# Optimization experiments

Measured on AMD Instinct MI355X. Metric: run time of the kernel, lower is better.

## Reference

```python
import jax, jax.numpy as jnp
import numpy as np
from jax import lax

# db4 decomposition low-pass filter (pywt convention, ascending index)
DEC_LO = np.array([-0.010597401784997278, 0.032883011666982945, 0.030841381835986965,
                   -0.18703481171888114, -0.02798376941698385, 0.6308807679295904,
                   0.7148465705525415, 0.23037781330885523], dtype=np.float32)
L = 8
REC_LO = DEC_LO[::-1].copy()
DEC_HI = (REC_LO * ((-1.0) ** (np.arange(L) + 1))).astype(np.float32)
REC_HI = DEC_HI[::-1].copy()


def _dwt_last(x, lo, hi):
    """Single-level DWT along last axis, pywt 'symmetric' mode.
    Returns (cA, cD), each (..., (N+L-1)//2)."""
    ext = jnp.pad(x, [(0, 0)] * (x.ndim - 1) + [(L - 1, L - 1)], mode='symmetric')[..., 1:]
    z = ext.reshape(-1, 1, ext.shape[-1])
    # correlation with flipped filter == true convolution
    k = jnp.stack([lo[::-1], hi[::-1]])[:, None, :]  # (2,1,L)
    y = lax.conv_general_dilated(z, k, (2,), 'VALID', dimension_numbers=('NCH', 'OIH', 'NCH'))
    y = y.reshape(x.shape[:-1] + (2, y.shape[-1]))
    return y[..., 0, :], y[..., 1, :]


def _idwt_last(cA, cD, lo, hi):
    """Single-level inverse DWT along last axis (pywt upsampling convolution)."""
    n = cA.shape[-1]
    up = jnp.zeros(cA.shape[:-1] + (2, 2 * n - 1), cA.dtype)
    up = up.at[..., 0, ::2].set(cA).at[..., 1, ::2].set(cD)
    z = up.reshape(-1, 2, 2 * n - 1)
    k = jnp.stack([lo[::-1], hi[::-1]])[None, :, :]  # (1,2,L) -> sum of lo/hi branches
    y = lax.conv_general_dilated(z, k, (1,), [(L - 1, L - 1)], dimension_numbers=('NCH', 'OIH', 'NCH'))
    y = y[:, 0, L - 2: 2 * n]  # length 2n - L + 2
    return y.reshape(cA.shape[:-1] + (2 * n - L + 2,))


def dwt2d(x):
    lo, hi = jnp.asarray(DEC_LO), jnp.asarray(DEC_HI)
    a, d = _dwt_last(x, lo, hi)                       # along W
    aa, da = _dwt_last(a.swapaxes(-1, -2), lo, hi)    # along H
    ad, dd = _dwt_last(d.swapaxes(-1, -2), lo, hi)
    LL = aa.swapaxes(-1, -2)
    LH = da.swapaxes(-1, -2)   # cH: detail along H, approx along W
    HL = ad.swapaxes(-1, -2)   # cV: approx along H, detail along W
    HH = dd.swapaxes(-1, -2)
    return LL, LH, HL, HH


def idwt2d(LL, LH, HL, HH):
    lo, hi = jnp.asarray(REC_LO), jnp.asarray(REC_HI)
    a = _idwt_last(LL.swapaxes(-1, -2), LH.swapaxes(-1, -2), lo, hi).swapaxes(-1, -2)  # along H
    d = _idwt_last(HL.swapaxes(-1, -2), HH.swapaxes(-1, -2), lo, hi).swapaxes(-1, -2)
    return _idwt_last(a, d, lo, hi)  # along W


def attention_weight(x, c1w, c1b, c2w, gamma, beta, rmean, rvar):
    """x: (b, w, c, h). Max/mean pool over dim 1, 1x1 conv 2->1, depthwise conv1d
    over c channels, BatchNorm1d (eval), sigmoid gate."""
    feat = jnp.stack([x.max(axis=1), x.mean(axis=1)], axis=1)  # (b,2,c,h)
    y = jnp.einsum('i,bich->bch', c1w.reshape(2), feat) + c1b[0]  # (b,c,h)
    C = y.shape[1]
    p = (c2w.shape[-1] - 1) // 2
    y = lax.conv_general_dilated(y, c2w, (1,), [(p, p)], feature_group_count=C,
                                 dimension_numbers=('NCH', 'OIH', 'NCH'))
    y = (y - rmean[:, None]) * lax.rsqrt(rvar[:, None] + 1e-5) * gamma[:, None] + beta[:, None]
    return x * jax.nn.sigmoid(y)[:, None]


def _forward(x, lh_c1w, lh_c1b, lh_c2w, lh_g, lh_b, lh_m, lh_v,
             hl_c1w, hl_c1b, hl_c2w, hl_g, hl_b, hl_m, hl_v):
    LL, LH, HL, HH = dwt2d(x)
    LHp = attention_weight(LH.transpose(0, 3, 1, 2), lh_c1w, lh_c1b, lh_c2w, lh_g, lh_b, lh_m, lh_v).transpose(0, 2, 3, 1)
    HLp = attention_weight(HL.transpose(0, 2, 1, 3), hl_c1w, hl_c1b, hl_c2w, hl_g, hl_b, hl_m, hl_v).transpose(0, 2, 1, 3)
    rec = idwt2d(LL, LHp, HLp, HH)
    H, W = x.shape[-2], x.shape[-1]
    return x + rec[..., :H, :W]


def setup_inputs() -> dict:
    key = jax.random.key(0)
    ks = jax.random.split(key, 16)
    B, C, H, W, K = 8, 64, 512, 512, 3
    d = {"x": jax.random.normal(ks[0], (B, C, H, W), dtype=jnp.float32)}
    for i, pre in enumerate(["lh", "hl"]):
        base = 1 + 7 * i
        d[pre + "_c1w"] = jax.random.normal(ks[base + 0], (1, 2, 1, 1), dtype=jnp.float32) * 0.5
        d[pre + "_c1b"] = jax.random.normal(ks[base + 1], (1,), dtype=jnp.float32) * 0.1
        d[pre + "_c2w"] = jax.random.normal(ks[base + 2], (C, 1, K), dtype=jnp.float32) * 0.3
        d[pre + "_g"] = jnp.ones((C,), dtype=jnp.float32)
        d[pre + "_b"] = jnp.zeros((C,), dtype=jnp.float32)
        d[pre + "_m"] = jax.random.normal(ks[base + 3], (C,), dtype=jnp.float32) * 0.1
        d[pre + "_v"] = jax.random.uniform(ks[base + 4], (C,), dtype=jnp.float32, minval=0.5, maxval=1.5)
    return d


def reference(x, lh_c1w, lh_c1b, lh_c2w, lh_g, lh_b, lh_m, lh_v,
              hl_c1w, hl_c1b, hl_c2w, hl_g, hl_b, hl_m, hl_v):
    return _forward(x, lh_c1w, lh_c1b, lh_c2w, lh_g, lh_b, lh_m, lh_v,
                    hl_c1w, hl_c1b, hl_c2w, hl_g, hl_b, hl_m, hl_v)
```

## Files before the change

### kernel.cpp

```cpp
#include <hip/hip_runtime.h>

typedef _Float16 h16;
typedef _Float16 h16x2 __attribute__((ext_vector_type(2)));
typedef _Float16 h16x4 __attribute__((ext_vector_type(4)));
typedef _Float16 h16x8 __attribute__((ext_vector_type(8)));
typedef float f32x4 __attribute__((ext_vector_type(4)));

#define N_IMG 512
#define C_CH  64
#define H_IN  512
#define W_IN  512
#define NC    259
#define PITH  264
#define S_IMGH ((size_t)NC * PITH)
#define NSB    ((size_t)N_IMG * S_IMGH)
#define GPIT  264
#define FSTRIP 17
#define LROWS  38

constexpr float DLO[8] = {
  -0.010597401784997278f,  0.032883011666982945f,  0.030841381835986965f, -0.18703481171888114f,
  -0.02798376941698385f,   0.6308807679295904f,    0.7148465705525415f,    0.23037781330885523f};
constexpr float DHI[8] = {
  -0.23037781330885523f,   0.7148465705525415f,   -0.6308807679295904f,   -0.02798376941698385f,
   0.18703481171888114f,   0.030841381835986965f, -0.032883011666982945f, -0.010597401784997278f};
constexpr float RLO[8] = {
   0.23037781330885523f,   0.7148465705525415f,    0.6308807679295904f,   -0.02798376941698385f,
  -0.18703481171888114f,   0.030841381835986965f,  0.032883011666982945f, -0.010597401784997278f};
constexpr float RHI[8] = {
  -0.010597401784997278f, -0.032883011666982945f,  0.030841381835986965f,  0.18703481171888114f,
  -0.02798376941698385f,  -0.6308807679295904f,    0.7148465705525415f,   -0.23037781330885523f};

__global__ __launch_bounds__(512) void k_fwd(const float* __restrict__ x,
                                             h16* __restrict__ wsh,
                                             float* __restrict__ stat) {
  __shared__ h16 sa16[LROWS * PITH];
  __shared__ h16 sd16[LROWS * PITH];
  const int p = blockIdx.x;
  const int w = (p & 7) * 1088 + (p >> 3);
  const int bc = w / FSTRIP;
  const int bx = w - bc * FSTRIP;
  const int h0 = bx * 16;
  const int hcount = min(16, NC - h0);
  const int nrows = 2 * hcount + 6;
  const int tid = threadIdx.x;
  const int wave = tid >> 6, lane = tid & 63;
  const float* xim = x + (size_t)bc * (H_IN * (size_t)W_IN);

  for (int j = wave; j < nrows; j += 8) {
    int r = 2 * h0 - 6 + j;
    r = r < 0 ? -r - 1 : (r >= H_IN ? 2 * H_IN - 1 - r : r);
    const float* xrow = xim + (size_t)r * W_IN;
    h16* saj = sa16 + j * PITH;
    h16* sdj = sd16 + j * PITH;
    const int base = lane ? 8 * lane - 8 : 0;
    const float4 q0 = *(const float4*)(xrow + base);
    const float4 q1 = *(const float4*)(xrow + base + 4);
    const float4 q2 = *(const float4*)(xrow + base + 8);
    const float4 q3 = *(const float4*)(xrow + base + 12);
    const float v[16] = {q0.x, q0.y, q0.z, q0.w, q1.x, q1.y, q1.z, q1.w,
                         q2.x, q2.y, q2.z, q2.w, q3.x, q3.y, q3.z, q3.w};
    float A[4], D[4];
    if (lane == 0) {
#pragma unroll
      for (int i = 0; i < 4; ++i) {
        float a = 0.f, d = 0.f;
#pragma unroll
        for (int m = 0; m < 8; ++m) {
          int pp = 2 * i + 1 - m; pp = pp < 0 ? -pp - 1 : pp;
          const float t = v[pp];
          a += DLO[m] * t; d += DHI[m] * t;
        }
        A[i] = a; D[i] = d;
      }
      h16x4 oa, od;
#pragma unroll
      for (int k = 0; k < 4; ++k) { oa[k] = (h16)A[k]; od[k] = (h16)D[k]; }
      *(h16x4*)(saj) = oa; *(h16x4*)(sdj) = od;
    } else {
#pragma unroll
      for (int k = 0; k < 4; ++k) {
        float a = 0.f, d = 0.f;
#pragma unroll
        for (int m = 0; m < 8; ++m) {
          const float t = v[2 * k + 9 - m];
          a += DLO[m] * t; d += DHI[m] * t;
        }
        A[k] = a; D[k] = d;
      }
      h16x4 oa, od;
#pragma unroll
      for (int k = 0; k < 4; ++k) { oa[k] = (h16)A[k]; od[k] = (h16)D[k]; }
      *(h16x4*)(saj + 4 * lane) = oa; *(h16x4*)(sdj + 4 * lane) = od;
      if (lane == 63) {
#pragma unroll
        for (int i = 256; i < 259; ++i) {
          float a = 0.f, d = 0.f;
#pragma unroll
          for (int m = 0; m < 8; ++m) {
            int pp = 2 * i + 1 - m; pp = pp >= 512 ? 1023 - pp : pp;
            const float t = v[pp - 496];
            a += DLO[m] * t; d += DHI[m] * t;
          }
          saj[i] = (h16)a; sdj[i] = (h16)d;
        }
      }
    }
  }
  __syncthreads();

  h16* __restrict__ LHp = wsh;
  h16* __restrict__ HLp = wsh + NSB;
  const size_t obase = (size_t)bc * S_IMGH;
  const int ntask = hcount * 65;
  float rlh[3][4], rhl[3][4];
#pragma unroll
  for (int slot = 0; slot < 3; ++slot) {
    const int task = tid + slot * 512;
    if (task < ntask) {
      const int dh = task / 65, pq = task - dh * 65;
      const int i0 = 4 * pq;
      float lh[4] = {0, 0, 0, 0}, hl[4] = {0, 0, 0, 0};
#pragma unroll
      for (int m = 0; m < 8; ++m) {
        const int j = 2 * dh + 7 - m;
        const h16x4 av = *(const h16x4*)(sa16 + j * PITH + i0);
        const h16x4 dv = *(const h16x4*)(sd16 + j * PITH + i0);
        lh[0] += DHI[m] * (float)av[0]; lh[1] += DHI[m] * (float)av[1];
        lh[2] += DHI[m] * (float)av[2]; lh[3] += DHI[m] * (float)av[3];
        hl[0] += DLO[m] * (float)dv[0]; hl[1] += DLO[m] * (float)dv[1];
        hl[2] += DLO[m] * (float)dv[2]; hl[3] += DLO[m] * (float)dv[3];
      }
      if (i0 == 256) { lh[3] = 0.f; hl[3] = 0.f; }
      const size_t ob = obase + (size_t)(h0 + dh) * PITH + i0;
      h16x4 o;
      o[0] = (h16)lh[0]; o[1] = (h16)lh[1]; o[2] = (h16)lh[2]; o[3] = (h16)lh[3];
      *(h16x4*)(LHp + ob) = o;
      o[0] = (h16)hl[0]; o[1] = (h16)hl[1]; o[2] = (h16)hl[2]; o[3] = (h16)hl[3];
      *(h16x4*)(HLp + ob) = o;
#pragma unroll
      for (int k = 0; k < 4; ++k) { rlh[slot][k] = lh[k]; rhl[slot][k] = hl[k]; }
    }
  }
  __syncthreads();

  float* scol = (float*)sa16;
  float* prmx = (float*)sd16;
  float* prsm = prmx + 1056;
#pragma unroll
  for (int slot = 0; slot < 3; ++slot) {
    const int task = tid + slot * 512;
    if (task < ntask) {
      const int dh = task / 65, pq = task - dh * 65;
      *(float4*)(scol + dh * 264 + 4 * pq) = {rhl[slot][0], rhl[slot][1], rhl[slot][2], rhl[slot][3]};
      const float m01 = fmaxf(rlh[slot][0], rlh[slot][1]);
      const float m23 = (pq == 64) ? rlh[slot][2] : fmaxf(rlh[slot][2], rlh[slot][3]);
      prmx[task] = fmaxf(m01, m23);
      prsm[task] = rlh[slot][0] + rlh[slot][1] + rlh[slot][2] + rlh[slot][3];
    }
  }
  __syncthreads();
  float* rsM = stat;
  float* rsS = stat + (size_t)N_IMG * 264;
  float* cpM = rsS + (size_t)N_IMG * 264;
  float* cpS = cpM + (size_t)N_IMG * FSTRIP * 264;
  for (int hh = wave; hh < hcount; hh += 8) {
    float m = prmx[hh * 65 + lane], s = prsm[hh * 65 + lane];
    if (lane == 0) { m = fmaxf(m, prmx[hh * 65 + 64]); s += prsm[hh * 65 + 64]; }
#pragma unroll
    for (int off = 32; off; off >>= 1) {
      m = fmaxf(m, __shfl_xor(m, off)); s += __shfl_xor(s, off);
    }
    if (lane == 0) {
      rsM[bc * 264 + h0 + hh] = m;
      rsS[bc * 264 + h0 + hh] = s;
    }
  }
  if (tid < 264) {
    float m = -3.4e38f, s = 0.f;
    for (int dh = 0; dh < hcount; ++dh) {
      const float vv = scol[dh * 264 + tid]; m = fmaxf(m, vv); s += vv;
    }
    const size_t cb = ((size_t)bc * FSTRIP + bx) * 264 + tid;
    cpM[cb] = m; cpS[cb] = s;
  }
}

__global__ __launch_bounds__(256) void k_gate(
    const float* __restrict__ stat, float* __restrict__ gout,
    const float* lc1w, const float* lc1b, const float* lc2w,
    const float* lg, const float* lb, const float* lm, const float* lv,
    const float* hc1w, const float* hc1b, const float* hc2w,
    const float* hg, const float* hb, const float* hm, const float* hv) {
  __shared__ float cmx[264], csm[264], y0a[264], y0b[264];
  const int bc = blockIdx.x;
  const int tid = threadIdx.x;
  const float* rsM = stat;
  const float* rsS = stat + (size_t)N_IMG * 264;
  const float* cpM = rsS + (size_t)N_IMG * 264;
  const float* cpS = cpM + (size_t)N_IMG * FSTRIP * 264;

  for (int col = tid; col < 264; col += 256) {
    float m = -3.4e38f, s = 0.f;
    for (int st = 0; st < FSTRIP; ++st) {
      const size_t cb = ((size_t)bc * FSTRIP + st) * 264 + col;
      m = fmaxf(m, cpM[cb]); s += cpS[cb];
    }
    cmx[col] = m; csm[col] = s;
  }
  __syncthreads();
  const float lw0 = lc1w[0], lw1 = lc1w[1], lbb0 = lc1b[0];
  const float hw0 = hc1w[0], hw1 = hc1w[1], hbb0 = hc1b[0];
  for (int idx = tid; idx < NC; idx += 256) {
    y0a[idx] = lw0 * rsM[bc * 264 + idx] + lw1 * (rsS[bc * 264 + idx] * (1.f / NC)) + lbb0;
    y0b[idx] = hw0 * cmx[idx] + hw1 * (csm[idx] * (1.f / NC)) + hbb0;
  }
  __syncthreads();
  const int c = bc & (C_CH - 1);
  const float lk0 = lc2w[c * 3], lk1 = lc2w[c * 3 + 1], lk2 = lc2w[c * 3 + 2];
  const float hk0 = hc2w[c * 3], hk1 = hc2w[c * 3 + 1], hk2 = hc2w[c * 3 + 2];
  const float lsc = rsqrtf(lv[c] + 1e-5f) * lg[c], lmu = lm[c], lbe = lb[c];
  const float hsc = rsqrtf(hv[c] + 1e-5f) * hg[c], hmu = hm[c], hbe = hb[c];
  for (int idx = tid; idx < NC; idx += 256) {
    float a = idx > 0 ? y0a[idx - 1] : 0.f;
    float b = y0a[idx];
    float d = idx < NC - 1 ? y0a[idx + 1] : 0.f;
    float y = lk0 * a + lk1 * b + lk2 * d;
    y = (y - lmu) * lsc + lbe;
    gout[(size_t)bc * GPIT + idx] = 1.f / (1.f + expf(-y)) - 1.f;

    a = idx > 0 ? y0b[idx - 1] : 0.f;
    b = y0b[idx];
    d = idx < NC - 1 ? y0b[idx + 1] : 0.f;
    y = hk0 * a + hk1 * b + hk2 * d;
    y = (y - hmu) * hsc + hbe;
    gout[(size_t)N_IMG * GPIT + (size_t)bc * GPIT + idx] = 1.f / (1.f + expf(-y)) - 1.f;
  }
}

__global__ __launch_bounds__(512) void k_inv(const h16* __restrict__ wsh,
                                             const float* __restrict__ gbuf,
                                             const float* __restrict__ x,
                                             float* __restrict__ out) {
  __shared__ float sB[7][PITH], sC[7][PITH];
  __shared__ float a2[8][PITH], d2[8][PITH];
  __shared__ float sghl[PITH];
  const int p = blockIdx.x;
  const int w = (p & 7) * 4096 + (p >> 3);
  const int bc = w >> 6;
  const int t0 = (w & 63) * 8;
  const int u0 = t0 >> 1;
  const int tid = threadIdx.x;
  const h16* LHh = wsh       + (size_t)bc * S_IMGH;
  const h16* HLh = wsh + NSB + (size_t)bc * S_IMGH;
  const float* glh = gbuf + (size_t)bc * GPIT;
  const float* ghl = gbuf + (size_t)N_IMG * GPIT + (size_t)bc * GPIT;

  if (tid < 66) *(float4*)(sghl + 4 * tid) = *(const float4*)(ghl + 4 * tid);

  for (int q = tid; q < 7 * 33; q += 512) {
    const int j = q / 33, b8 = (q - j * 33) * 8;
    const int u = u0 + j;
    const float gl = glh[u];
    const size_t rb = (size_t)u * PITH + b8;
    const h16x8 Bv = *(const h16x8*)(LHh + rb);
    const h16x8 Cv = *(const h16x8*)(HLh + rb);
    float4 f0 = {(float)Bv[0] * gl, (float)Bv[1] * gl, (float)Bv[2] * gl, (float)Bv[3] * gl};
    float4 f1 = {(float)Bv[4] * gl, (float)Bv[5] * gl, (float)Bv[6] * gl, (float)Bv[7] * gl};
    *(float4*)(&sB[j][b8]) = f0; *(float4*)(&sB[j][b8 + 4]) = f1;
    f0 = {(float)Cv[0], (float)Cv[1], (float)Cv[2], (float)Cv[3]};
    f1 = {(float)Cv[4], (float)Cv[5], (float)Cv[6], (float)Cv[7]};
    *(float4*)(&sC[j][b8]) = f0; *(float4*)(&sC[j][b8 + 4]) = f1;
  }
  __syncthreads();

  for (int task = tid; task < 8 * 132; task += 512) {
    const int dt = task / 132, pq = task - dt * 132;
    const int i = 2 * pq;
    const int par = dt & 1, lj0 = dt >> 1;
    float ax = 0.f, ay = 0.f, dx_ = 0.f, dy_ = 0.f;
#pragma unroll
    for (int jj = 0; jj < 4; ++jj) {
      const int lj = lj0 + 3 - jj;
      const float rh = par ? RHI[1 + 2 * jj] : RHI[2 * jj];
      const float rl = par ? RLO[1 + 2 * jj] : RLO[2 * jj];
      const float2 b_ = *(const float2*)(&sB[lj][i]);
      const float2 c_ = *(const float2*)(&sC[lj][i]);
      ax += b_.x * rh; ay += b_.y * rh;
      dx_ += c_.x * rl; dy_ += c_.y * rl;
    }
    *(float2*)(&a2[dt][i]) = {ax, ay};
    *(float2*)(&d2[dt][i]) = {sghl[i] * dx_, sghl[i + 1] * dy_};
  }
  __syncthreads();

  for (int task = tid; task < 8 * 128; task += 512) {
    const int dt = task >> 7, r = task & 127;
    const int q = 2 * r;
    const float a_[5] = {a2[dt][q], a2[dt][q + 1], a2[dt][q + 2], a2[dt][q + 3], a2[dt][q + 4]};
    const float d_[5] = {d2[dt][q], d2[dt][q + 1], d2[dt][q + 2], d2[dt][q + 3], d2[dt][q + 4]};
    float vv[4];
#pragma unroll
    for (int k = 0; k < 4; ++k) {
      float s = 0.f;
      const int base = k >> 1, par = k & 1;
#pragma unroll
      for (int jj = 0; jj < 4; ++jj)
        s += a_[base + 3 - jj] * RLO[par + 2 * jj] + d_[base + 3 - jj] * RHI[par + 2 * jj];
      vv[k] = s;
    }
    const size_t orow = ((size_t)bc * H_IN + (size_t)(t0 + dt)) * W_IN + 4 * r;
    const f32x4 xv = __builtin_nontemporal_load((const f32x4*)(x + orow));
    f32x4 ov;
    ov.x = 2.f * xv.x + vv[0]; ov.y = 2.f * xv.y + vv[1];
    ov.z = 2.f * xv.z + vv[2]; ov.w = 2.f * xv.w + vv[3];
    __builtin_nontemporal_store(ov, (f32x4*)(out + orow));
  }
}

extern "C" void kernel_launch(void* const* d_in, const int* in_sizes, int n_in,
                              void* d_out, int out_size, void* d_ws, size_t ws_size,
                              hipStream_t stream) {
  const float* x = (const float*)d_in[0];
  h16* wsh = (h16*)d_ws;
  float* statf = (float*)(wsh + 2 * NSB);
  float* gbuf = statf + 2 * (size_t)N_IMG * 264 + 2 * (size_t)N_IMG * FSTRIP * 264;
  float* out = (float*)d_out;

  k_fwd<<<dim3(FSTRIP * N_IMG), 512, 0, stream>>>(x, wsh, statf);
  k_gate<<<dim3(N_IMG), 256, 0, stream>>>(
      statf, gbuf,
      (const float*)d_in[1], (const float*)d_in[2], (const float*)d_in[3],
      (const float*)d_in[4], (const float*)d_in[5], (const float*)d_in[6], (const float*)d_in[7],
      (const float*)d_in[8], (const float*)d_in[9], (const float*)d_in[10],
      (const float*)d_in[11], (const float*)d_in[12], (const float*)d_in[13], (const float*)d_in[14]);
  k_inv<<<dim3(64 * N_IMG), 512, 0, stream>>>(wsh, gbuf, x, out);
}
```

Measured before the change: 405.8 us.

## Interleave LH/HL subbands in fp16 pairs and use packed half math

Stores the two detail subbands interleaved as half2 pairs in one workspace buffer and one shared tile. Forward and inverse filtering now run with packed fp16 vector multiply-adds and fdot2 instead of scalar fp32. The inverse kernel handles 16 output rows per block instead of 8, with intermediates kept in fp16 shared memory. This is meant to cut ALU work, shared memory footprint and the number of load instructions, and to reuse halo rows across more outputs. In exchange, fp16 accumulation lowers precision of the intermediate sums.

```diff
diff --git a/kernel.cpp b/kernel.cpp
--- a/kernel.cpp
+++ b/kernel.cpp
@@ -6,14 +6,21 @@
 typedef _Float16 h16x8 __attribute__((ext_vector_type(8)));
 typedef float f32x4 __attribute__((ext_vector_type(4)));
 
+#if __has_builtin(__builtin_amdgcn_fdot2)
+#define FDOT2(a, b, c) __builtin_amdgcn_fdot2((a), (b), (c), false)
+#else
+static __device__ __forceinline__ float FDOT2(h16x2 a, h16x2 b, float c) {
+  return c + (float)a[0] * (float)b[0] + (float)a[1] * (float)b[1];
+}
+#endif
+
 #define N_IMG 512
 #define C_CH  64
 #define H_IN  512
 #define W_IN  512
 #define NC    259
-#define PITH  264
-#define S_IMGH ((size_t)NC * PITH)
-#define NSB    ((size_t)N_IMG * S_IMGH)
+#define PITP  528
+#define S2    ((size_t)NC * PITP)
 #define GPIT  264
 #define FSTRIP 17
 #define LROWS  38
@@ -34,8 +41,7 @@
 __global__ __launch_bounds__(512) void k_fwd(const float* __restrict__ x,
                                              h16* __restrict__ wsh,
                                              float* __restrict__ stat) {
-  __shared__ h16 sa16[LROWS * PITH];
-  __shared__ h16 sd16[LROWS * PITH];
+  __shared__ h16 sad[LROWS * PITP];
   const int p = blockIdx.x;
   const int w = (p & 7) * 1088 + (p >> 3);
   const int bc = w / FSTRIP;
@@ -51,8 +57,7 @@
     int r = 2 * h0 - 6 + j;
     r = r < 0 ? -r - 1 : (r >= H_IN ? 2 * H_IN - 1 - r : r);
     const float* xrow = xim + (size_t)r * W_IN;
-    h16* saj = sa16 + j * PITH;
-    h16* sdj = sd16 + j * PITH;
+    h16* sj = sad + j * PITP;
     const int base = lane ? 8 * lane - 8 : 0;
     const float4 q0 = *(const float4*)(xrow + base);
     const float4 q1 = *(const float4*)(xrow + base + 4);
@@ -60,8 +65,8 @@
     const float4 q3 = *(const float4*)(xrow + base + 12);
     const float v[16] = {q0.x, q0.y, q0.z, q0.w, q1.x, q1.y, q1.z, q1.w,
                          q2.x, q2.y, q2.z, q2.w, q3.x, q3.y, q3.z, q3.w};
-    float A[4], D[4];
     if (lane == 0) {
+      h16x8 o;
 #pragma unroll
       for (int i = 0; i < 4; ++i) {
         float a = 0.f, d = 0.f;
@@ -71,13 +76,11 @@
           const float t = v[pp];
           a += DLO[m] * t; d += DHI[m] * t;
         }
-        A[i] = a; D[i] = d;
-      }
-      h16x4 oa, od;
-#pragma unroll
-      for (int k = 0; k < 4; ++k) { oa[k] = (h16)A[k]; od[k] = (h16)D[k]; }
-      *(h16x4*)(saj) = oa; *(h16x4*)(sdj) = od;
+        o[2 * i] = (h16)a; o[2 * i + 1] = (h16)d;
+      }
+      *(h16x8*)(sj) = o;
     } else {
+      h16x8 o;
 #pragma unroll
       for (int k = 0; k < 4; ++k) {
         float a = 0.f, d = 0.f;
@@ -86,12 +89,9 @@
           const float t = v[2 * k + 9 - m];
           a += DLO[m] * t; d += DHI[m] * t;
         }
-        A[k] = a; D[k] = d;
-      }
-      h16x4 oa, od;
-#pragma unroll
-      for (int k = 0; k < 4; ++k) { oa[k] = (h16)A[k]; od[k] = (h16)D[k]; }
-      *(h16x4*)(saj + 4 * lane) = oa; *(h16x4*)(sdj + 4 * lane) = od;
+        o[2 * k] = (h16)a; o[2 * k + 1] = (h16)d;
+      }
+      *(h16x8*)(sj + 8 * lane) = o;
       if (lane == 63) {
 #pragma unroll
         for (int i = 256; i < 259; ++i) {
@@ -102,61 +102,64 @@
             const float t = v[pp - 496];
             a += DLO[m] * t; d += DHI[m] * t;
           }
-          saj[i] = (h16)a; sdj[i] = (h16)d;
+          h16x2 o2; o2[0] = (h16)a; o2[1] = (h16)d;
+          *(h16x2*)(sj + 2 * i) = o2;
         }
       }
     }
   }
   __syncthreads();
 
-  h16* __restrict__ LHp = wsh;
-  h16* __restrict__ HLp = wsh + NSB;
-  const size_t obase = (size_t)bc * S_IMGH;
-  const int ntask = hcount * 65;
+  const size_t obase = (size_t)bc * S2;
+  const int ntask = hcount * 66;
   float rlh[3][4], rhl[3][4];
 #pragma unroll
   for (int slot = 0; slot < 3; ++slot) {
     const int task = tid + slot * 512;
     if (task < ntask) {
-      const int dh = task / 65, pq = task - dh * 65;
-      const int i0 = 4 * pq;
-      float lh[4] = {0, 0, 0, 0}, hl[4] = {0, 0, 0, 0};
+      const int dh = task / 66, pq = task - dh * 66;
+      h16x2 a0 = {0, 0}, a1 = {0, 0}, a2_ = {0, 0}, a3 = {0, 0};
 #pragma unroll
       for (int m = 0; m < 8; ++m) {
         const int j = 2 * dh + 7 - m;
-        const h16x4 av = *(const h16x4*)(sa16 + j * PITH + i0);
-        const h16x4 dv = *(const h16x4*)(sd16 + j * PITH + i0);
-        lh[0] += DHI[m] * (float)av[0]; lh[1] += DHI[m] * (float)av[1];
-        lh[2] += DHI[m] * (float)av[2]; lh[3] += DHI[m] * (float)av[3];
-        hl[0] += DLO[m] * (float)dv[0]; hl[1] += DLO[m] * (float)dv[1];
-        hl[2] += DLO[m] * (float)dv[2]; hl[3] += DLO[m] * (float)dv[3];
-      }
-      if (i0 == 256) { lh[3] = 0.f; hl[3] = 0.f; }
-      const size_t ob = obase + (size_t)(h0 + dh) * PITH + i0;
-      h16x4 o;
-      o[0] = (h16)lh[0]; o[1] = (h16)lh[1]; o[2] = (h16)lh[2]; o[3] = (h16)lh[3];
-      *(h16x4*)(LHp + ob) = o;
-      o[0] = (h16)hl[0]; o[1] = (h16)hl[1]; o[2] = (h16)hl[2]; o[3] = (h16)hl[3];
-      *(h16x4*)(HLp + ob) = o;
-#pragma unroll
-      for (int k = 0; k < 4; ++k) { rlh[slot][k] = lh[k]; rhl[slot][k] = hl[k]; }
-    }
-  }
-  __syncthreads();
-
-  float* scol = (float*)sa16;
-  float* prmx = (float*)sd16;
+        const h16x8 pr = *(const h16x8*)(sad + j * PITP + 8 * pq);
+        const h16x2 cf = {(h16)DHI[m], (h16)DLO[m]};
+        const h16x2 p0 = {pr[0], pr[1]}, p1 = {pr[2], pr[3]};
+        const h16x2 p2 = {pr[4], pr[5]}, p3 = {pr[6], pr[7]};
+        a0 += cf * p0; a1 += cf * p1; a2_ += cf * p2; a3 += cf * p3;
+      }
+      if (pq == 64) { a3 = (h16x2){0, 0}; }
+      if (pq == 65) { a0 = a1 = a2_ = a3 = (h16x2){0, 0}; }
+      h16x8 o = {a0[0], a0[1], a1[0], a1[1], a2_[0], a2_[1], a3[0], a3[1]};
+      *(h16x8*)(wsh + obase + (size_t)(h0 + dh) * PITP + 8 * pq) = o;
+      rlh[slot][0] = (float)a0[0]; rlh[slot][1] = (float)a1[0];
+      rlh[slot][2] = (float)a2_[0]; rlh[slot][3] = (float)a3[0];
+      rhl[slot][0] = (float)a0[1]; rhl[slot][1] = (float)a1[1];
+      rhl[slot][2] = (float)a2_[1]; rhl[slot][3] = (float)a3[1];
+    }
+  }
+  __syncthreads();
+
+  float* scol = (float*)sad;
+  float* prmx = scol + 16 * 264;
   float* prsm = prmx + 1056;
 #pragma unroll
   for (int slot = 0; slot < 3; ++slot) {
     const int task = tid + slot * 512;
     if (task < ntask) {
-      const int dh = task / 65, pq = task - dh * 65;
-      *(float4*)(scol + dh * 264 + 4 * pq) = {rhl[slot][0], rhl[slot][1], rhl[slot][2], rhl[slot][3]};
-      const float m01 = fmaxf(rlh[slot][0], rlh[slot][1]);
-      const float m23 = (pq == 64) ? rlh[slot][2] : fmaxf(rlh[slot][2], rlh[slot][3]);
-      prmx[task] = fmaxf(m01, m23);
-      prsm[task] = rlh[slot][0] + rlh[slot][1] + rlh[slot][2] + rlh[slot][3];
+      const int dh = task / 66, pq = task - dh * 66;
+      if (pq < 66) {
+        *(float4*)(scol + dh * 264 + 4 * pq) =
+            {rhl[slot][0], rhl[slot][1], rhl[slot][2], rhl[slot][3]};
+      }
+      if (pq == 65) {
+        prmx[task] = -3.4e38f; prsm[task] = 0.f;
+      } else {
+        const float m01 = fmaxf(rlh[slot][0], rlh[slot][1]);
+        const float m23 = (pq == 64) ? rlh[slot][2] : fmaxf(rlh[slot][2], rlh[slot][3]);
+        prmx[task] = fmaxf(m01, m23);
+        prsm[task] = rlh[slot][0] + rlh[slot][1] + rlh[slot][2] + rlh[slot][3];
+      }
     }
   }
   __syncthreads();
@@ -165,8 +168,11 @@
   float* cpM = rsS + (size_t)N_IMG * 264;
   float* cpS = cpM + (size_t)N_IMG * FSTRIP * 264;
   for (int hh = wave; hh < hcount; hh += 8) {
-    float m = prmx[hh * 65 + lane], s = prsm[hh * 65 + lane];
-    if (lane == 0) { m = fmaxf(m, prmx[hh * 65 + 64]); s += prsm[hh * 65 + 64]; }
+    float m = prmx[hh * 66 + lane], s = prsm[hh * 66 + lane];
+    if (lane == 0) {
+      m = fmaxf(m, fmaxf(prmx[hh * 66 + 64], prmx[hh * 66 + 65]));
+      s += prsm[hh * 66 + 64] + prsm[hh * 66 + 65];
+    }
 #pragma unroll
     for (int off = 32; off; off >>= 1) {
       m = fmaxf(m, __shfl_xor(m, off)); s += __shfl_xor(s, off);
@@ -242,71 +248,76 @@
                                              const float* __restrict__ gbuf,
                                              const float* __restrict__ x,
                                              float* __restrict__ out) {
-  __shared__ float sB[7][PITH], sC[7][PITH];
-  __shared__ float a2[8][PITH], d2[8][PITH];
-  __shared__ float sghl[PITH];
+  __shared__ h16 sBC[11 * PITP];
+  __shared__ h16 ad2[16 * PITP];
+  __shared__ h16 sghl16[264];
   const int p = blockIdx.x;
-  const int w = (p & 7) * 4096 + (p >> 3);
-  const int bc = w >> 6;
-  const int t0 = (w & 63) * 8;
+  const int w = (p & 7) * 2048 + (p >> 3);
+  const int bc = w >> 5;
+  const int t0 = (w & 31) * 16;
   const int u0 = t0 >> 1;
   const int tid = threadIdx.x;
-  const h16* LHh = wsh       + (size_t)bc * S_IMGH;
-  const h16* HLh = wsh + NSB + (size_t)bc * S_IMGH;
+  const h16* sub = wsh + (size_t)bc * S2;
   const float* glh = gbuf + (size_t)bc * GPIT;
   const float* ghl = gbuf + (size_t)N_IMG * GPIT + (size_t)bc * GPIT;
 
-  if (tid < 66) *(float4*)(sghl + 4 * tid) = *(const float4*)(ghl + 4 * tid);
-
-  for (int q = tid; q < 7 * 33; q += 512) {
-    const int j = q / 33, b8 = (q - j * 33) * 8;
+  if (tid < 264) sghl16[tid] = (h16)ghl[tid];
+
+  for (int t = tid; t < 11 * 66; t += 512) {
+    const int j = t / 66, pq = t - j * 66;
     const int u = u0 + j;
-    const float gl = glh[u];
-    const size_t rb = (size_t)u * PITH + b8;
-    const h16x8 Bv = *(const h16x8*)(LHh + rb);
-    const h16x8 Cv = *(const h16x8*)(HLh + rb);
-    float4 f0 = {(float)Bv[0] * gl, (float)Bv[1] * gl, (float)Bv[2] * gl, (float)Bv[3] * gl};
-    float4 f1 = {(float)Bv[4] * gl, (float)Bv[5] * gl, (float)Bv[6] * gl, (float)Bv[7] * gl};
-    *(float4*)(&sB[j][b8]) = f0; *(float4*)(&sB[j][b8 + 4]) = f1;
-    f0 = {(float)Cv[0], (float)Cv[1], (float)Cv[2], (float)Cv[3]};
-    f1 = {(float)Cv[4], (float)Cv[5], (float)Cv[6], (float)Cv[7]};
-    *(float4*)(&sC[j][b8]) = f0; *(float4*)(&sC[j][b8 + 4]) = f1;
-  }
-  __syncthreads();
-
-  for (int task = tid; task < 8 * 132; task += 512) {
+    const h16 glH = (h16)glh[u];
+    const h16x2 cf = {glH, (h16)1.0f};
+    const h16x8 pr = *(const h16x8*)(sub + (size_t)u * PITP + 8 * pq);
+    h16x2 r0 = cf * (h16x2){pr[0], pr[1]};
+    h16x2 r1 = cf * (h16x2){pr[2], pr[3]};
+    h16x2 r2 = cf * (h16x2){pr[4], pr[5]};
+    h16x2 r3 = cf * (h16x2){pr[6], pr[7]};
+    h16x8 o = {r0[0], r0[1], r1[0], r1[1], r2[0], r2[1], r3[0], r3[1]};
+    *(h16x8*)(sBC + j * PITP + 8 * pq) = o;
+  }
+  __syncthreads();
+
+  for (int task = tid; task < 16 * 132; task += 512) {
     const int dt = task / 132, pq = task - dt * 132;
-    const int i = 2 * pq;
     const int par = dt & 1, lj0 = dt >> 1;
-    float ax = 0.f, ay = 0.f, dx_ = 0.f, dy_ = 0.f;
+    h16x2 acc0 = {0, 0}, acc1 = {0, 0};
 #pragma unroll
     for (int jj = 0; jj < 4; ++jj) {
       const int lj = lj0 + 3 - jj;
-      const float rh = par ? RHI[1 + 2 * jj] : RHI[2 * jj];
-      const float rl = par ? RLO[1 + 2 * jj] : RLO[2 * jj];
-      const float2 b_ = *(const float2*)(&sB[lj][i]);
-      const float2 c_ = *(const float2*)(&sC[lj][i]);
-      ax += b_.x * rh; ay += b_.y * rh;
-      dx_ += c_.x * rl; dy_ += c_.y * rl;
-    }
-    *(float2*)(&a2[dt][i]) = {ax, ay};
-    *(float2*)(&d2[dt][i]) = {sghl[i] * dx_, sghl[i + 1] * dy_};
-  }
-  __syncthreads();
-
-  for (int task = tid; task < 8 * 128; task += 512) {
+      const h16x2 cf = {(h16)(par ? RHI[1 + 2 * jj] : RHI[2 * jj]),
+                        (h16)(par ? RLO[1 + 2 * jj] : RLO[2 * jj])};
+      const h16x4 pr = *(const h16x4*)(sBC + lj * PITP + 4 * pq);
+      acc0 += cf * (h16x2){pr[0], pr[1]};
+      acc1 += cf * (h16x2){pr[2], pr[3]};
+    }
+    const h16x2 g2 = *(const h16x2*)(sghl16 + 2 * pq);
+    const h16x2 cg0 = {(h16)1.0f, g2[0]};
+    const h16x2 cg1 = {(h16)1.0f, g2[1]};
+    acc0 *= cg0; acc1 *= cg1;
+    h16x4 o = {acc0[0], acc0[1], acc1[0], acc1[1]};
+    *(h16x4*)(ad2 + dt * PITP + 4 * pq) = o;
+  }
+  __syncthreads();
+
+  for (int task = tid; task < 16 * 128; task += 512) {
     const int dt = task >> 7, r = task & 127;
-    const int q = 2 * r;
-    const float a_[5] = {a2[dt][q], a2[dt][q + 1], a2[dt][q + 2], a2[dt][q + 3], a2[dt][q + 4]};
-    const float d_[5] = {d2[dt][q], d2[dt][q + 1], d2[dt][q + 2], d2[dt][q + 3], d2[dt][q + 4]};
+    const h16* row = ad2 + dt * PITP + 4 * r;
+    const h16x4 w0 = *(const h16x4*)(row);
+    const h16x4 w1 = *(const h16x4*)(row + 4);
+    const h16x2 w2 = *(const h16x2*)(row + 8);
+    const h16x2 P[5] = {{w0[0], w0[1]}, {w0[2], w0[3]},
+                        {w1[0], w1[1]}, {w1[2], w1[3]}, w2};
     float vv[4];
 #pragma unroll
     for (int k = 0; k < 4; ++k) {
+      const int base = k >> 1, par = k & 1;
       float s = 0.f;
-      const int base = k >> 1, par = k & 1;
-#pragma unroll
-      for (int jj = 0; jj < 4; ++jj)
-        s += a_[base + 3 - jj] * RLO[par + 2 * jj] + d_[base + 3 - jj] * RHI[par + 2 * jj];
+#pragma unroll
+      for (int jj = 0; jj < 4; ++jj) {
+        const h16x2 cf = {(h16)RLO[par + 2 * jj], (h16)RHI[par + 2 * jj]};
+        s = FDOT2(P[base + 3 - jj], cf, s);
+      }
       vv[k] = s;
     }
     const size_t orow = ((size_t)bc * H_IN + (size_t)(t0 + dt)) * W_IN + 4 * r;
@@ -323,7 +334,7 @@
                               hipStream_t stream) {
   const float* x = (const float*)d_in[0];
   h16* wsh = (h16*)d_ws;
-  float* statf = (float*)(wsh + 2 * NSB);
+  float* statf = (float*)(wsh + (size_t)N_IMG * S2);
   float* gbuf = statf + 2 * (size_t)N_IMG * 264 + 2 * (size_t)N_IMG * FSTRIP * 264;
   float* out = (float*)d_out;
 
@@ -334,5 +345,5 @@
       (const float*)d_in[4], (const float*)d_in[5], (const float*)d_in[6], (const float*)d_in[7],
       (const float*)d_in[8], (const float*)d_in[9], (const float*)d_in[10],
       (const float*)d_in[11], (const float*)d_in[12], (const float*)d_in[13], (const float*)d_in[14]);
-  k_inv<<<dim3(64 * N_IMG), 512, 0, stream>>>(wsh, gbuf, x, out);
-}
+  k_inv<<<dim3(32 * N_IMG), 512, 0, stream>>>(wsh, gbuf, x, out);
+}
```

Measured after the change: 370.3 us (median of 2 runs). 8.7% less time.
